# Optimization experiments

Measured on AMD Instinct MI355X. Metric: run time of the kernel, lower is better.

The kernel has to match this reference:

```python
import jax, jax.numpy as jnp
import numpy as np

N, E, G, ND, H, C, L = 100000, 640000, 1000, 128, 128, 10, 4
ATOMS_PER_GRAPH = 100  # N = G * ATOMS_PER_GRAPH
NEG_SLOPE = 0.01  # nn.LeakyReLU default


def setup_inputs() -> dict:
    key = jax.random.key(0)
    ks = jax.random.split(key, 16)
    s = 0.05
    return {
        "node_attr": jax.random.normal(ks[0], (N, ND), jnp.float32),
        "edge_index": jax.random.randint(ks[1], (2, E), 0, N, jnp.int64),
        "num_atoms": jnp.full((G,), ATOMS_PER_GRAPH, dtype=jnp.int64),
        "enc_W": jax.random.normal(ks[2], (ND, H), jnp.float32) * s,
        "enc_b": jnp.zeros((H,), jnp.float32),
        "gcn_W": jax.random.normal(ks[3], (L, H, H), jnp.float32) * s,
        "gcn_b": jnp.zeros((L, H), jnp.float32),
        "r_W1": jax.random.normal(ks[4], (H, H), jnp.float32) * s,
        "r_b1": jnp.zeros((H,), jnp.float32),
        "r_W2": jax.random.normal(ks[5], (H, H), jnp.float32) * s,
        "r_b2": jnp.zeros((H,), jnp.float32),
        "s_W1": jax.random.normal(ks[6], (H, H), jnp.float32) * s,
        "s_b1": jnp.zeros((H,), jnp.float32),
        "s_W2": jax.random.normal(ks[7], (H, H), jnp.float32) * s,
        "s_b2": jnp.zeros((H,), jnp.float32),
        "fin_W": jax.random.normal(ks[8], (H, C), jnp.float32) * s,
        "fin_b": jnp.zeros((C,), jnp.float32),
    }


def _leaky(x):
    return jnp.where(x > 0, x, NEG_SLOPE * x)


def reference(node_attr, edge_index, num_atoms, enc_W, enc_b, gcn_W, gcn_b,
              r_W1, r_b1, r_W2, r_b2, s_W1, s_b1, s_W2, s_b2, fin_W, fin_b):
    dst, src = edge_index[0], edge_index[1]
    # degree normalization constant across layers: deg(i) = in-edge count, divide by deg+1
    deg = jax.ops.segment_sum(jnp.ones((E,), node_attr.dtype), dst, num_segments=N)
    inv_deg = 1.0 / (deg + 1.0)  # [N]

    x = node_attr @ enc_W + enc_b  # [N, H]
    for l in range(L):
        h = x @ gcn_W[l] + gcn_b[l]
        agg = jax.ops.segment_sum(h[src], dst, num_segments=N)  # scatter_sum over dst
        x = (h + agg) * inv_deg[:, None]

    # GateMLP: ReLuMLP(x) * SigmoidMLP(x)
    r = _leaky(_leaky(x @ r_W1 + r_b1) @ r_W2 + r_b2)
    g = jax.nn.sigmoid(_leaky(x @ s_W1 + s_b1) @ s_W2 + s_b2)
    x = r * g  # [N, H]

    # graph pooling: scatter_mean over graph ids
    graph_mask = jnp.repeat(jnp.arange(G), num_atoms, total_repeat_length=N)
    gsum = jax.ops.segment_sum(x, graph_mask, num_segments=G)
    cnt = jax.ops.segment_sum(jnp.ones((N,), x.dtype), graph_mask, num_segments=G)
    graph_attr = gsum / jnp.maximum(cnt, 1.0)[:, None]  # [G, H]
    return graph_attr @ fin_W + fin_b  # [G, C]
```

## Files before the change

kernel.cpp:

```cpp
#include <hip/hip_runtime.h>
#include <hip/hip_bf16.h>
#include <cstddef>
#include <cstdint>

#define CAP 40
#define LEAK 0.01f

typedef __attribute__((ext_vector_type(8))) short short8v;
typedef __attribute__((ext_vector_type(4))) float float4v;

__device__ __forceinline__ unsigned short f2bf(float f) {
    uint32_t u = __float_as_uint(f);
    uint32_t r = (u + 0x7FFFu + ((u >> 16) & 1u)) >> 16;
    return (unsigned short)r;
}
__device__ __forceinline__ float bf2f(unsigned short s) {
    return __uint_as_float(((uint32_t)s) << 16);
}
__device__ __forceinline__ short8v frag_from_pairs(uint32_t p0, uint32_t p1,
                                                   uint32_t p2, uint32_t p3) {
    union { uint32_t u[4]; short8v v; } c;
    c.u[0] = p0; c.u[1] = p1; c.u[2] = p2; c.u[3] = p3;
    return c.v;
}

__global__ void build_buckets(const int* __restrict__ ei, int E_,
                              int* __restrict__ cnt, int* __restrict__ bucket) {
    int e = (blockIdx.x * 256 + threadIdx.x) * 4;
    if (e >= E_) return;
    if (e + 4 <= E_) {
        int4 d4 = *(const int4*)&ei[e];
        int4 s4 = *(const int4*)&ei[(size_t)E_ + e];
        int p0 = atomicAdd(&cnt[d4.x], 1);
        int p1 = atomicAdd(&cnt[d4.y], 1);
        int p2 = atomicAdd(&cnt[d4.z], 1);
        int p3 = atomicAdd(&cnt[d4.w], 1);
        if (p0 < CAP) bucket[(size_t)d4.x * CAP + p0] = s4.x;
        if (p1 < CAP) bucket[(size_t)d4.y * CAP + p1] = s4.y;
        if (p2 < CAP) bucket[(size_t)d4.z * CAP + p2] = s4.z;
        if (p3 < CAP) bucket[(size_t)d4.w * CAP + p3] = s4.w;
    } else {
        for (; e < E_; ++e) {
            int d = ei[e], s = ei[(size_t)E_ + e];
            int p = atomicAdd(&cnt[d], 1);
            if (p < CAP) bucket[(size_t)d * CAP + p] = s;
        }
    }
}

__global__ void pack_w(const float* __restrict__ enc, const float* __restrict__ gcn,
                       const float* __restrict__ rw1, const float* __restrict__ rw2,
                       const float* __restrict__ sw1, const float* __restrict__ sw2,
                       unsigned short* __restrict__ p) {
    int m = blockIdx.x >> 3;
    int idx = (blockIdx.x & 7) * 256 + threadIdx.x;
    const float* W;
    switch (m) {
        case 0: W = enc; break;
        case 1: case 2: case 3: case 4: W = gcn + (size_t)(m - 1) * 16384; break;
        case 5: W = rw1; break;
        case 6: W = rw2; break;
        case 7: W = sw1; break;
        default: W = sw2; break;
    }
    int n = idx & 127;
    int fg = (idx >> 7) & 3;
    int kc = idx >> 9;
    short8v v;
#pragma unroll
    for (int j = 0; j < 8; ++j)
        v[j] = (short)f2bf(W[(size_t)(kc * 32 + fg * 8 + j) * 128 + n]);
    *(short8v*)(p + (size_t)m * 16384 + (size_t)idx * 8) = v;
}

__device__ __forceinline__ void load_wf(const unsigned short* __restrict__ Wpack,
                                        int w, int fr, int fg, short8v wf[2][4]) {
    const short8v* Wp = (const short8v*)Wpack;
#pragma unroll
    for (int t = 0; t < 2; ++t)
#pragma unroll
        for (int kc = 0; kc < 4; ++kc)
            wf[t][kc] = Wp[(kc * 4 + fg) * 128 + w * 32 + t * 16 + fr];
}

__device__ __forceinline__ void mfma_tile(const unsigned short* As, int fr, int fg,
                                          const short8v wf[2][4], float4v acc[4][2]) {
#pragma unroll
    for (int m = 0; m < 4; ++m) {
        acc[m][0] = (float4v){0.f, 0.f, 0.f, 0.f};
        acc[m][1] = (float4v){0.f, 0.f, 0.f, 0.f};
    }
#pragma unroll
    for (int kc = 0; kc < 4; ++kc) {
        short8v a[4];
#pragma unroll
        for (int m = 0; m < 4; ++m) {
            int row = m * 16 + fr;
            int cb = (kc * 64 + fg * 16) ^ ((row & 7) << 4);
            a[m] = *(const short8v*)((const char*)As + row * 256 + cb);
        }
#pragma unroll
        for (int m = 0; m < 4; ++m) {
            acc[m][0] = __builtin_amdgcn_mfma_f32_16x16x32_bf16(a[m], wf[0][kc], acc[m][0], 0, 0, 0);
            acc[m][1] = __builtin_amdgcn_mfma_f32_16x16x32_bf16(a[m], wf[1][kc], acc[m][1], 0, 0, 0);
        }
    }
}

__global__ __launch_bounds__(256) void gemm_enc(const float* __restrict__ Ain,
                                                const unsigned short* __restrict__ Wpack,
                                                const float* __restrict__ bias,
                                                unsigned short* __restrict__ Cout, int M) {
    __shared__ unsigned short As[64 * 128];
    const int tid = threadIdx.x;
    const int lane = tid & 63;
    const int w = tid >> 6;
    const int row0 = blockIdx.x * 64;
    const int fr = lane & 15;
    const int fg = lane >> 4;

    short8v wf[2][4];
    load_wf(Wpack, w, fr, fg, wf);

    {
        const int r = tid >> 2;
        const int cg = tid & 3;
        const int row = row0 + r;
        char* lbase = (char*)As + r * 256;
        const float* Ap = Ain + (size_t)row * 128 + cg * 32;
#pragma unroll
        for (int i = 0; i < 4; ++i) {
            short8v v = {0, 0, 0, 0, 0, 0, 0, 0};
            if (row < M) {
                float4v p = *(const float4v*)(Ap + i * 8);
                float4v q = *(const float4v*)(Ap + i * 8 + 4);
                v[0] = (short)f2bf(p[0]); v[1] = (short)f2bf(p[1]);
                v[2] = (short)f2bf(p[2]); v[3] = (short)f2bf(p[3]);
                v[4] = (short)f2bf(q[0]); v[5] = (short)f2bf(q[1]);
                v[6] = (short)f2bf(q[2]); v[7] = (short)f2bf(q[3]);
            }
            int cb = (cg * 64 + i * 16) ^ ((r & 7) << 4);
            *(short8v*)(lbase + cb) = v;
        }
    }
    __syncthreads();

    float4v acc[4][2];
    mfma_tile(As, fr, fg, wf, acc);

#pragma unroll
    for (int t = 0; t < 2; ++t) {
        const int col = w * 32 + t * 16 + fr;
        const float bv = bias[col];
#pragma unroll
        for (int m = 0; m < 4; ++m)
#pragma unroll
            for (int q = 0; q < 4; ++q) {
                int row = row0 + m * 16 + fg * 4 + q;
                if (row < M) Cout[(size_t)row * 128 + col] = f2bf(acc[m][t][q] + bv);
            }
    }
}

__device__ __forceinline__ void acc8(float a[8], uint4 v, float m) {
    a[0] = fmaf(m, bf2f((unsigned short)(v.x & 0xffff)), a[0]);
    a[1] = fmaf(m, bf2f((unsigned short)(v.x >> 16)), a[1]);
    a[2] = fmaf(m, bf2f((unsigned short)(v.y & 0xffff)), a[2]);
    a[3] = fmaf(m, bf2f((unsigned short)(v.y >> 16)), a[3]);
    a[4] = fmaf(m, bf2f((unsigned short)(v.z & 0xffff)), a[4]);
    a[5] = fmaf(m, bf2f((unsigned short)(v.z >> 16)), a[5]);
    a[6] = fmaf(m, bf2f((unsigned short)(v.w & 0xffff)), a[6]);
    a[7] = fmaf(m, bf2f((unsigned short)(v.w >> 16)), a[7]);
}

__global__ __launch_bounds__(256, 4) void gcn_fused(const unsigned short* __restrict__ x,
                                                    const int* __restrict__ bucket,
                                                    const int* __restrict__ cnt,
                                                    const unsigned short* __restrict__ Wpack,
                                                    const float* __restrict__ bias,
                                                    unsigned short* __restrict__ xout,
                                                    int Nn) {
    __shared__ unsigned short As[64 * 128];
    const int tid = threadIdx.x;
    const int lane = tid & 63;
    const int w = tid >> 6;
    const int row0 = blockIdx.x * 64;
    const int fr = lane & 15;
    const int fg = lane >> 4;
    const int l16 = lane & 15;
    const int g = lane >> 4;
    const int gl = lane & 48;
    const char* xb = (const char*)x;

    int cfull = 0;
    if (lane < 16) {
        int gn = row0 + w * 16 + lane;
        if (gn >= Nn) gn = Nn - 1;
        cfull = cnt[gn];
    }
    uint4 own[4];
    int2 pre[4];
#pragma unroll
    for (int p = 0; p < 4; ++p) {
        int gn = row0 + w * 16 + p * 4 + g;
        if (gn >= Nn) gn = Nn - 1;
        own[p] = *(const uint4*)(xb + (size_t)gn * 256 + l16 * 16);
        pre[p] = *(const int2*)&bucket[(size_t)gn * CAP + 2 * l16];
    }

#pragma unroll
    for (int p = 0; p < 4; ++p) {
        const int n = p * 4 + g;
        const int r = w * 16 + n;
        const int dfull = __shfl(cfull, n);
        const float id = 1.0f / (float)(dfull + 1);
        const int d = min(dfull, CAP);
        const int dm = min(d, 32);

        float a[8];
        {
            uint4 o = own[p];
            a[0] = bf2f((unsigned short)(o.x & 0xffff));
            a[1] = bf2f((unsigned short)(o.x >> 16));
            a[2] = bf2f((unsigned short)(o.y & 0xffff));
            a[3] = bf2f((unsigned short)(o.y >> 16));
            a[4] = bf2f((unsigned short)(o.z & 0xffff));
            a[5] = bf2f((unsigned short)(o.z >> 16));
            a[6] = bf2f((unsigned short)(o.w & 0xffff));
            a[7] = bf2f((unsigned short)(o.w >> 16));
        }

        for (int j = 0; j < dm; j += 4) {
            int sl = gl + (j >> 1);
            int s0 = __shfl(pre[p].x, sl);
            int s1 = __shfl(pre[p].y, sl);
            int s2 = __shfl(pre[p].x, sl + 1);
            int s3 = __shfl(pre[p].y, sl + 1);
            s0 = min(max(s0, 0), Nn - 1);
            s1 = min(max(s1, 0), Nn - 1);
            s2 = min(max(s2, 0), Nn - 1);
            s3 = min(max(s3, 0), Nn - 1);
            uint4 v0 = *(const uint4*)(xb + (size_t)s0 * 256 + l16 * 16);
            uint4 v1 = *(const uint4*)(xb + (size_t)s1 * 256 + l16 * 16);
            uint4 v2 = *(const uint4*)(xb + (size_t)s2 * 256 + l16 * 16);
            uint4 v3 = *(const uint4*)(xb + (size_t)s3 * 256 + l16 * 16);
            acc8(a, v0, (j + 0 < d) ? 1.f : 0.f);
            acc8(a, v1, (j + 1 < d) ? 1.f : 0.f);
            acc8(a, v2, (j + 2 < d) ? 1.f : 0.f);
            acc8(a, v3, (j + 3 < d) ? 1.f : 0.f);
        }
        if (d > 32) {
            int gn = row0 + r; if (gn >= Nn) gn = Nn - 1;
            for (int j = 32; j < d; ++j) {
                int s = bucket[(size_t)gn * CAP + j];
                uint4 v = *(const uint4*)(xb + (size_t)s * 256 + l16 * 16);
                acc8(a, v, 1.f);
            }
        }

#pragma unroll
        for (int i = 0; i < 8; ++i) a[i] *= id;
        uint4 o;
        o.x = (uint32_t)f2bf(a[0]) | ((uint32_t)f2bf(a[1]) << 16);
        o.y = (uint32_t)f2bf(a[2]) | ((uint32_t)f2bf(a[3]) << 16);
        o.z = (uint32_t)f2bf(a[4]) | ((uint32_t)f2bf(a[5]) << 16);
        o.w = (uint32_t)f2bf(a[6]) | ((uint32_t)f2bf(a[7]) << 16);
        *(uint4*)((char*)As + r * 256 + ((l16 * 16) ^ ((r & 7) << 4))) = o;
    }

    short8v wf[2][4];
    load_wf(Wpack, w, fr, fg, wf);
    __syncthreads();

    float4v acc[4][2];
    mfma_tile(As, fr, fg, wf, acc);

#pragma unroll
    for (int t = 0; t < 2; ++t) {
        const int col = w * 32 + t * 16 + fr;
        const float bv = bias[col];
#pragma unroll
        for (int m = 0; m < 4; ++m)
#pragma unroll
            for (int q = 0; q < 4; ++q) {
                int row = row0 + m * 16 + fg * 4 + q;
                if (row < Nn) xout[(size_t)row * 128 + col] = f2bf(acc[m][t][q] + bv);
            }
    }
}

__global__ __launch_bounds__(512, 4) void gate_fused(const unsigned short* __restrict__ x,
                                                     const unsigned short* __restrict__ wpack,
                                                     const float* __restrict__ rb1,
                                                     const float* __restrict__ rb2,
                                                     const float* __restrict__ sb1,
                                                     const float* __restrict__ sb2,
                                                     unsigned short* __restrict__ out, int M) {
    __shared__ unsigned short Ws[2 * 128 * 128];
    const int tid = threadIdx.x;
    const int lane = tid & 63;
    const int w = tid >> 6;
    const int l16 = lane & 15;
    const int fg = lane >> 4;
    const int row0 = blockIdx.x * 128 + w * 16;

    int xr = row0 + l16;
    if (xr >= M) xr = M - 1;
    short8v xbf[4];
#pragma unroll
    for (int kc = 0; kc < 4; ++kc)
        xbf[kc] = *(const short8v*)(x + (size_t)xr * 128 + kc * 32 + fg * 8);

    const short8v* WL = (const short8v*)Ws;
    uint32_t upR[8][2], upS[8][2];

#define STAGE2(mi0, mi1)                                                      \
    {                                                                         \
        const short8v* s0 = (const short8v*)(wpack + (size_t)(mi0) * 16384);  \
        const short8v* s1 = (const short8v*)(wpack + (size_t)(mi1) * 16384);  \
        short8v* dst = (short8v*)Ws;                                          \
        _Pragma("unroll") for (int i = 0; i < 4; ++i)                         \
            dst[i * 512 + tid] = s0[i * 512 + tid];                           \
        _Pragma("unroll") for (int i = 0; i < 4; ++i)                         \
            dst[2048 + i * 512 + tid] = s1[i * 512 + tid];                    \
    }

#define PASS1(OFS, BIAS, UP)                                                  \
    _Pragma("unroll") for (int nt = 0; nt < 8; ++nt) {                        \
        float4v acc = (float4v){0.f, 0.f, 0.f, 0.f};                          \
        _Pragma("unroll") for (int kc = 0; kc < 4; ++kc)                      \
            acc = __builtin_amdgcn_mfma_f32_16x16x32_bf16(                    \
                WL[(OFS) + (kc * 4 + fg) * 128 + nt * 16 + l16], xbf[kc], acc, 0, 0, 0); \
        _Pragma("unroll") for (int q = 0; q < 4; ++q) {                       \
            float v = acc[q] + (BIAS)[nt * 16 + fg * 4 + q];                  \
            acc[q] = v > 0.f ? v : LEAK * v;                                  \
        }                                                                     \
        UP[nt][0] = (uint32_t)f2bf(acc[0]) | ((uint32_t)f2bf(acc[1]) << 16);  \
        UP[nt][1] = (uint32_t)f2bf(acc[2]) | ((uint32_t)f2bf(acc[3]) << 16);  \
    }

#define MKUF(UP, UF)                                                          \
    _Pragma("unroll") for (int kc = 0; kc < 4; ++kc) {                        \
        uint32_t pr0, pr1, pr2, pr3;                                          \
        {                                                                     \
            int srcl = (((2 * fg + 0) & 3) << 4) + l16;                       \
            uint32_t lo = __shfl((int)UP[2 * kc][0], srcl);                   \
            uint32_t hi = __shfl((int)UP[2 * kc + 1][0], srcl);               \
            pr0 = (fg & 2) ? hi : lo;                                         \
            lo = __shfl((int)UP[2 * kc][1], srcl);                            \
            hi = __shfl((int)UP[2 * kc + 1][1], srcl);                        \
            pr1 = (fg & 2) ? hi : lo;                                         \
        }                                                                     \
        {                                                                     \
            int srcl = (((2 * fg + 1) & 3) << 4) + l16;                       \
            uint32_t lo = __shfl((int)UP[2 * kc][0], srcl);                   \
            uint32_t hi = __shfl((int)UP[2 * kc + 1][0], srcl);               \
            pr2 = (fg & 2) ? hi : lo;                                         \
            lo = __shfl((int)UP[2 * kc][1], srcl);                            \
            hi = __shfl((int)UP[2 * kc + 1][1], srcl);                        \
            pr3 = (fg & 2) ? hi : lo;                                         \
        }                                                                     \
        UF[kc] = frag_from_pairs(pr0, pr1, pr2, pr3);                         \
    }

    STAGE2(5, 7);
    __syncthreads();
    PASS1(0, rb1, upR);
    PASS1(2048, sb1, upS);
    __syncthreads();

    STAGE2(6, 8);
    __syncthreads();

    short8v uf[4];
    MKUF(upR, uf);
    float4v rf[8];
#pragma unroll
    for (int t2 = 0; t2 < 8; ++t2) {
        float4v acc = (float4v){0.f, 0.f, 0.f, 0.f};
#pragma unroll
        for (int kc = 0; kc < 4; ++kc)
            acc = __builtin_amdgcn_mfma_f32_16x16x32_bf16(
                uf[kc], WL[(kc * 4 + fg) * 128 + t2 * 16 + l16], acc, 0, 0, 0);
        const float bv = rb2[t2 * 16 + l16];
#pragma unroll
        for (int q = 0; q < 4; ++q) {
            float v = acc[q] + bv;
            rf[t2][q] = v > 0.f ? v : LEAK * v;
        }
    }

    MKUF(upS, uf);
#pragma unroll
    for (int t2 = 0; t2 < 8; ++t2) {
        float4v acc = (float4v){0.f, 0.f, 0.f, 0.f};
#pragma unroll
        for (int kc = 0; kc < 4; ++kc)
            acc = __builtin_amdgcn_mfma_f32_16x16x32_bf16(
                uf[kc], WL[2048 + (kc * 4 + fg) * 128 + t2 * 16 + l16], acc, 0, 0, 0);
        const float bv = sb2[t2 * 16 + l16];
#pragma unroll
        for (int q = 0; q < 4; ++q) {
            int row = row0 + fg * 4 + q;
            if (row < M) {
                float gg = 1.f / (1.f + __expf(-(acc[q] + bv)));
                out[(size_t)row * 128 + t2 * 16 + l16] = f2bf(gg * rf[t2][q]);
            }
        }
    }
#undef STAGE2
#undef PASS1
#undef MKUF
}

__global__ void scan_atoms(const int* __restrict__ na, int* __restrict__ goff, int G_) {
    __shared__ int sh[1024];
    int t = threadIdx.x;
    int v = (t < G_) ? na[t] : 0;
    sh[t] = v;
    __syncthreads();
    for (int ofs = 1; ofs < 1024; ofs <<= 1) {
        int u = (t >= ofs) ? sh[t - ofs] : 0;
        __syncthreads();
        sh[t] += u;
        __syncthreads();
    }
    if (t == 0) goff[0] = 0;
    if (t < G_) goff[t + 1] = sh[t];
}

__global__ void pool(const unsigned short* __restrict__ x, const int* __restrict__ goff,
                     float* __restrict__ gattr, int G_) {
    int g = blockIdx.x * 2 + (threadIdx.x >> 7);
    if (g >= G_) return;
    int d = threadIdx.x & 127;
    int a0 = goff[g], a1 = goff[g + 1];
    float s0 = 0.f, s1 = 0.f, s2 = 0.f, s3 = 0.f;
    int a = a0;
    for (; a + 4 <= a1; a += 4) {
        s0 += bf2f(x[(size_t)(a + 0) * 128 + d]);
        s1 += bf2f(x[(size_t)(a + 1) * 128 + d]);
        s2 += bf2f(x[(size_t)(a + 2) * 128 + d]);
        s3 += bf2f(x[(size_t)(a + 3) * 128 + d]);
    }
    for (; a < a1; ++a) s0 += bf2f(x[(size_t)a * 128 + d]);
    float s = (s0 + s1) + (s2 + s3);
    float c = (float)max(a1 - a0, 1);
    gattr[(size_t)g * 128 + d] = s / c;
}

__global__ void final_gemm(const float* __restrict__ gattr, const float* __restrict__ fW,
                           const float* __restrict__ fb, float* __restrict__ out,
                           int G_, int C_) {
    int i = blockIdx.x * 256 + threadIdx.x;
    if (i >= G_ * C_) return;
    int g = i / C_, c = i % C_;
    const float* row = gattr + (size_t)g * 128;
    float s = fb[c];
    for (int k = 0; k < 128; ++k) s = fmaf(row[k], fW[k * C_ + c], s);
    out[i] = s;
}

extern "C" void kernel_launch(void* const* d_in, const int* in_sizes, int n_in,
                              void* d_out, int out_size, void* d_ws, size_t ws_size,
                              hipStream_t stream) {
    const float* node_attr = (const float*)d_in[0];
    const int* edge_index  = (const int*)d_in[1];
    const int* num_atoms   = (const int*)d_in[2];
    const float* enc_W = (const float*)d_in[3];
    const float* enc_b = (const float*)d_in[4];
    const float* gcn_W = (const float*)d_in[5];
    const float* gcn_b = (const float*)d_in[6];
    const float* r_W1 = (const float*)d_in[7];
    const float* r_b1 = (const float*)d_in[8];
    const float* r_W2 = (const float*)d_in[9];
    const float* r_b2 = (const float*)d_in[10];
    const float* s_W1 = (const float*)d_in[11];
    const float* s_b1 = (const float*)d_in[12];
    const float* s_W2 = (const float*)d_in[13];
    const float* s_b2 = (const float*)d_in[14];
    const float* fin_W = (const float*)d_in[15];
    const float* fin_b = (const float*)d_in[16];
    float* out = (float*)d_out;

    const int N_ = in_sizes[0] / 128;
    const int E_ = in_sizes[1] / 2;
    const int G_ = in_sizes[2];
    const int C_ = in_sizes[16];

    size_t off = 0;
    auto alloc = [&](size_t bytes) -> void* {
        void* p = (char*)d_ws + off;
        off += (bytes + 255) & ~(size_t)255;
        return p;
    };
    unsigned short* bx = (unsigned short*)alloc((size_t)N_ * 128 * 2);
    unsigned short* bh = (unsigned short*)alloc((size_t)N_ * 128 * 2);
    int* bucket = (int*)alloc((size_t)N_ * CAP * 4);
    int* cnt    = (int*)alloc((size_t)N_ * 4);
    unsigned short* wpack = (unsigned short*)alloc((size_t)9 * 16384 * 2);
    int* goff   = (int*)alloc((size_t)(G_ + 1) * 4);
    float* gattr = (float*)alloc((size_t)G_ * 128 * 4);
    (void)ws_size; (void)n_in; (void)out_size;

    const int gemm_grid = (N_ + 63) / 64;

    hipMemsetAsync(cnt, 0, (size_t)N_ * 4, stream);
    build_buckets<<<(E_ / 4 + 255) / 256, 256, 0, stream>>>(edge_index, E_, cnt, bucket);
    pack_w<<<72, 256, 0, stream>>>(enc_W, gcn_W, r_W1, r_W2, s_W1, s_W2, wpack);
    scan_atoms<<<1, 1024, 0, stream>>>(num_atoms, goff, G_);

    gemm_enc<<<gemm_grid, 256, 0, stream>>>(node_attr, wpack, enc_b, bx, N_);

    unsigned short* cur = bx;
    unsigned short* nxt = bh;
    for (int l = 0; l < 4; ++l) {
        gcn_fused<<<gemm_grid, 256, 0, stream>>>(cur, bucket, cnt,
                                                 wpack + (size_t)(1 + l) * 16384,
                                                 gcn_b + (size_t)l * 128, nxt, N_);
        unsigned short* t = cur; cur = nxt; nxt = t;
    }

    gate_fused<<<(N_ + 127) / 128, 512, 0, stream>>>(cur, wpack, r_b1, r_b2, s_b1, s_b2,
                                                     nxt, N_);

    pool<<<(G_ + 1) / 2, 256, 0, stream>>>(nxt, goff, gattr, G_);
    final_gemm<<<(G_ * C_ + 255) / 256, 256, 0, stream>>>(gattr, fin_W, fin_b, out, G_, C_);
}
```

Baseline: 297.5 us.

## Prefetch neighbor gathers across nodes and shrink gate kernel shared memory

```diff
diff --git a/kernel.cpp b/kernel.cpp
--- a/kernel.cpp
+++ b/kernel.cpp
@@ -173,6 +173,26 @@
     a[7] = fmaf(m, bf2f((unsigned short)(v.w >> 16)), a[7]);
 }
 
+__device__ __forceinline__ void issue8(const char* __restrict__ xb, int2 prep,
+                                       int gl, int l16, int Nn, int jb, uint4 V[8]) {
+    const int sl = gl + (jb >> 1);
+    int s[8];
+    s[0] = __shfl(prep.x, sl);     s[1] = __shfl(prep.y, sl);
+    s[2] = __shfl(prep.x, sl + 1); s[3] = __shfl(prep.y, sl + 1);
+    s[4] = __shfl(prep.x, sl + 2); s[5] = __shfl(prep.y, sl + 2);
+    s[6] = __shfl(prep.x, sl + 3); s[7] = __shfl(prep.y, sl + 3);
+#pragma unroll
+    for (int i = 0; i < 8; ++i) {
+        int ss = min(max(s[i], 0), Nn - 1);
+        V[i] = *(const uint4*)(xb + (size_t)ss * 256 + l16 * 16);
+    }
+}
+
+__device__ __forceinline__ void consume8(float a[8], const uint4 V[8], int jb, int d) {
+#pragma unroll
+    for (int i = 0; i < 8; ++i) acc8(a, V[i], (jb + i < d) ? 1.f : 0.f);
+}
+
 __global__ __launch_bounds__(256, 4) void gcn_fused(const unsigned short* __restrict__ x,
                                                     const int* __restrict__ bucket,
                                                     const int* __restrict__ cnt,
@@ -208,65 +228,61 @@
         pre[p] = *(const int2*)&bucket[(size_t)gn * CAP + 2 * l16];
     }
 
-#pragma unroll
-    for (int p = 0; p < 4; ++p) {
-        const int n = p * 4 + g;
-        const int r = w * 16 + n;
-        const int dfull = __shfl(cfull, n);
-        const float id = 1.0f / (float)(dfull + 1);
-        const int d = min(dfull, CAP);
-        const int dm = min(d, 32);
-
-        float a[8];
-        {
-            uint4 o = own[p];
-            a[0] = bf2f((unsigned short)(o.x & 0xffff));
-            a[1] = bf2f((unsigned short)(o.x >> 16));
-            a[2] = bf2f((unsigned short)(o.y & 0xffff));
-            a[3] = bf2f((unsigned short)(o.y >> 16));
-            a[4] = bf2f((unsigned short)(o.z & 0xffff));
-            a[5] = bf2f((unsigned short)(o.z >> 16));
-            a[6] = bf2f((unsigned short)(o.w & 0xffff));
-            a[7] = bf2f((unsigned short)(o.w >> 16));
-        }
-
-        for (int j = 0; j < dm; j += 4) {
-            int sl = gl + (j >> 1);
-            int s0 = __shfl(pre[p].x, sl);
-            int s1 = __shfl(pre[p].y, sl);
-            int s2 = __shfl(pre[p].x, sl + 1);
-            int s3 = __shfl(pre[p].y, sl + 1);
-            s0 = min(max(s0, 0), Nn - 1);
-            s1 = min(max(s1, 0), Nn - 1);
-            s2 = min(max(s2, 0), Nn - 1);
-            s3 = min(max(s3, 0), Nn - 1);
-            uint4 v0 = *(const uint4*)(xb + (size_t)s0 * 256 + l16 * 16);
-            uint4 v1 = *(const uint4*)(xb + (size_t)s1 * 256 + l16 * 16);
-            uint4 v2 = *(const uint4*)(xb + (size_t)s2 * 256 + l16 * 16);
-            uint4 v3 = *(const uint4*)(xb + (size_t)s3 * 256 + l16 * 16);
-            acc8(a, v0, (j + 0 < d) ? 1.f : 0.f);
-            acc8(a, v1, (j + 1 < d) ? 1.f : 0.f);
-            acc8(a, v2, (j + 2 < d) ? 1.f : 0.f);
-            acc8(a, v3, (j + 3 < d) ? 1.f : 0.f);
-        }
-        if (d > 32) {
-            int gn = row0 + r; if (gn >= Nn) gn = Nn - 1;
-            for (int j = 32; j < d; ++j) {
-                int s = bucket[(size_t)gn * CAP + j];
-                uint4 v = *(const uint4*)(xb + (size_t)s * 256 + l16 * 16);
-                acc8(a, v, 1.f);
-            }
-        }
-
-#pragma unroll
-        for (int i = 0; i < 8; ++i) a[i] *= id;
-        uint4 o;
-        o.x = (uint32_t)f2bf(a[0]) | ((uint32_t)f2bf(a[1]) << 16);
-        o.y = (uint32_t)f2bf(a[2]) | ((uint32_t)f2bf(a[3]) << 16);
-        o.z = (uint32_t)f2bf(a[4]) | ((uint32_t)f2bf(a[5]) << 16);
-        o.w = (uint32_t)f2bf(a[6]) | ((uint32_t)f2bf(a[7]) << 16);
-        *(uint4*)((char*)As + r * 256 + ((l16 * 16) ^ ((r & 7) << 4))) = o;
-    }
+    uint4 VA[8], VB[8];
+
+#define DO_PASS(P, V)                                                          \
+    {                                                                          \
+        const int n = (P) * 4 + g;                                             \
+        const int r = w * 16 + n;                                              \
+        const int dfull = __shfl(cfull, n);                                    \
+        const float id = 1.0f / (float)(dfull + 1);                            \
+        const int d = min(dfull, CAP);                                         \
+        float a[8];                                                            \
+        {                                                                      \
+            uint4 o = own[P];                                                  \
+            a[0] = bf2f((unsigned short)(o.x & 0xffff));                       \
+            a[1] = bf2f((unsigned short)(o.x >> 16));                          \
+            a[2] = bf2f((unsigned short)(o.y & 0xffff));                       \
+            a[3] = bf2f((unsigned short)(o.y >> 16));                          \
+            a[4] = bf2f((unsigned short)(o.z & 0xffff));                       \
+            a[5] = bf2f((unsigned short)(o.z >> 16));                          \
+            a[6] = bf2f((unsigned short)(o.w & 0xffff));                       \
+            a[7] = bf2f((unsigned short)(o.w >> 16));                          \
+        }                                                                      \
+        consume8(a, V, 0, d);                                                  \
+        if (d > 8) {                                                           \
+            const int dm = min(d, 32);                                         \
+            for (int jb = 8; jb < dm; jb += 8) {                               \
+                issue8(xb, pre[P], gl, l16, Nn, jb, V);                        \
+                consume8(a, V, jb, d);                                         \
+            }                                                                  \
+            if (d > 32) {                                                      \
+                int gn = row0 + r; if (gn >= Nn) gn = Nn - 1;                  \
+                for (int j = 32; j < d; ++j) {                                 \
+                    int s = bucket[(size_t)gn * CAP + j];                      \
+                    uint4 v = *(const uint4*)(xb + (size_t)s * 256 + l16 * 16);\
+                    acc8(a, v, 1.f);                                           \
+                }                                                              \
+            }                                                                  \
+        }                                                                      \
+        _Pragma("unroll") for (int i = 0; i < 8; ++i) a[i] *= id;              \
+        uint4 o;                                                               \
+        o.x = (uint32_t)f2bf(a[0]) | ((uint32_t)f2bf(a[1]) << 16);             \
+        o.y = (uint32_t)f2bf(a[2]) | ((uint32_t)f2bf(a[3]) << 16);             \
+        o.z = (uint32_t)f2bf(a[4]) | ((uint32_t)f2bf(a[5]) << 16);             \
+        o.w = (uint32_t)f2bf(a[6]) | ((uint32_t)f2bf(a[7]) << 16);             \
+        *(uint4*)((char*)As + r * 256 + ((l16 * 16) ^ ((r & 7) << 4))) = o;    \
+    }
+
+    issue8(xb, pre[0], gl, l16, Nn, 0, VA);
+    issue8(xb, pre[1], gl, l16, Nn, 0, VB);
+    DO_PASS(0, VA);
+    issue8(xb, pre[2], gl, l16, Nn, 0, VA);
+    DO_PASS(1, VB);
+    issue8(xb, pre[3], gl, l16, Nn, 0, VB);
+    DO_PASS(2, VA);
+    DO_PASS(3, VB);
+#undef DO_PASS
 
     short8v wf[2][4];
     load_wf(Wpack, w, fr, fg, wf);
@@ -296,13 +312,12 @@
                                                      const float* __restrict__ sb1,
                                                      const float* __restrict__ sb2,
                                                      unsigned short* __restrict__ out, int M) {
-    __shared__ unsigned short Ws[2 * 128 * 128];
+    __shared__ unsigned short Ws[128 * 128];
     const int tid = threadIdx.x;
     const int lane = tid & 63;
-    const int w = tid >> 6;
     const int l16 = lane & 15;
     const int fg = lane >> 4;
-    const int row0 = blockIdx.x * 128 + w * 16;
+    const int row0 = blockIdx.x * 128 + (tid >> 6) * 16;
 
     int xr = row0 + l16;
     if (xr >= M) xr = M - 1;
@@ -314,23 +329,20 @@
     const short8v* WL = (const short8v*)Ws;
     uint32_t upR[8][2], upS[8][2];
 
-#define STAGE2(mi0, mi1)                                                      \
+#define STAGE(mi)                                                             \
     {                                                                         \
-        const short8v* s0 = (const short8v*)(wpack + (size_t)(mi0) * 16384);  \
-        const short8v* s1 = (const short8v*)(wpack + (size_t)(mi1) * 16384);  \
+        const short8v* src = (const short8v*)(wpack + (size_t)(mi) * 16384);  \
         short8v* dst = (short8v*)Ws;                                          \
         _Pragma("unroll") for (int i = 0; i < 4; ++i)                         \
-            dst[i * 512 + tid] = s0[i * 512 + tid];                           \
-        _Pragma("unroll") for (int i = 0; i < 4; ++i)                         \
-            dst[2048 + i * 512 + tid] = s1[i * 512 + tid];                    \
-    }
-
-#define PASS1(OFS, BIAS, UP)                                                  \
+            dst[i * 512 + tid] = src[i * 512 + tid];                          \
+    }
+
+#define PASS1(BIAS, UP)                                                       \
     _Pragma("unroll") for (int nt = 0; nt < 8; ++nt) {                        \
         float4v acc = (float4v){0.f, 0.f, 0.f, 0.f};                          \
         _Pragma("unroll") for (int kc = 0; kc < 4; ++kc)                      \
             acc = __builtin_amdgcn_mfma_f32_16x16x32_bf16(                    \
-                WL[(OFS) + (kc * 4 + fg) * 128 + nt * 16 + l16], xbf[kc], acc, 0, 0, 0); \
+                WL[(kc * 4 + fg) * 128 + nt * 16 + l16], xbf[kc], acc, 0, 0, 0); \
         _Pragma("unroll") for (int q = 0; q < 4; ++q) {                       \
             float v = acc[q] + (BIAS)[nt * 16 + fg * 4 + q];                  \
             acc[q] = v > 0.f ? v : LEAK * v;                                  \
@@ -363,14 +375,16 @@
         UF[kc] = frag_from_pairs(pr0, pr1, pr2, pr3);                         \
     }
 
-    STAGE2(5, 7);
+    STAGE(5);
     __syncthreads();
-    PASS1(0, rb1, upR);
-    PASS1(2048, sb1, upS);
+    PASS1(rb1, upR);
     __syncthreads();
-
-    STAGE2(6, 8);
+    STAGE(7);
     __syncthreads();
+    PASS1(sb1, upS);
+
+    const short8v* W2R = (const short8v*)(wpack + (size_t)6 * 16384);
+    const short8v* W2S = (const short8v*)(wpack + (size_t)8 * 16384);
 
     short8v uf[4];
     MKUF(upR, uf);
@@ -381,7 +395,7 @@
 #pragma unroll
         for (int kc = 0; kc < 4; ++kc)
             acc = __builtin_amdgcn_mfma_f32_16x16x32_bf16(
-                uf[kc], WL[(kc * 4 + fg) * 128 + t2 * 16 + l16], acc, 0, 0, 0);
+                uf[kc], W2R[(kc * 4 + fg) * 128 + t2 * 16 + l16], acc, 0, 0, 0);
         const float bv = rb2[t2 * 16 + l16];
 #pragma unroll
         for (int q = 0; q < 4; ++q) {
@@ -397,7 +411,7 @@
 #pragma unroll
         for (int kc = 0; kc < 4; ++kc)
             acc = __builtin_amdgcn_mfma_f32_16x16x32_bf16(
-                uf[kc], WL[2048 + (kc * 4 + fg) * 128 + t2 * 16 + l16], acc, 0, 0, 0);
+                uf[kc], W2S[(kc * 4 + fg) * 128 + t2 * 16 + l16], acc, 0, 0, 0);
         const float bv = sb2[t2 * 16 + l16];
 #pragma unroll
         for (int q = 0; q < 4; ++q) {
@@ -408,7 +422,7 @@
             }
         }
     }
-#undef STAGE2
+#undef STAGE
 #undef PASS1
 #undef MKUF
 }
```

After: 376.5 us. +26.6%, slower.

## Read gate MLP weights directly from global memory instead of LDS staging

Applied to the files above, without the earlier changes.

```diff
diff --git a/kernel.cpp b/kernel.cpp
--- a/kernel.cpp
+++ b/kernel.cpp
@@ -289,20 +289,18 @@
     }
 }
 
-__global__ __launch_bounds__(512, 4) void gate_fused(const unsigned short* __restrict__ x,
+__global__ __launch_bounds__(256, 4) void gate_fused(const unsigned short* __restrict__ x,
                                                      const unsigned short* __restrict__ wpack,
                                                      const float* __restrict__ rb1,
                                                      const float* __restrict__ rb2,
                                                      const float* __restrict__ sb1,
                                                      const float* __restrict__ sb2,
                                                      unsigned short* __restrict__ out, int M) {
-    __shared__ unsigned short Ws[2 * 128 * 128];
     const int tid = threadIdx.x;
     const int lane = tid & 63;
-    const int w = tid >> 6;
     const int l16 = lane & 15;
     const int fg = lane >> 4;
-    const int row0 = blockIdx.x * 128 + w * 16;
+    const int row0 = blockIdx.x * 64 + (tid >> 6) * 16;
 
     int xr = row0 + l16;
     if (xr >= M) xr = M - 1;
@@ -311,104 +309,96 @@
     for (int kc = 0; kc < 4; ++kc)
         xbf[kc] = *(const short8v*)(x + (size_t)xr * 128 + kc * 32 + fg * 8);
 
-    const short8v* WL = (const short8v*)Ws;
-    uint32_t upR[8][2], upS[8][2];
-
-#define STAGE2(mi0, mi1)                                                      \
-    {                                                                         \
-        const short8v* s0 = (const short8v*)(wpack + (size_t)(mi0) * 16384);  \
-        const short8v* s1 = (const short8v*)(wpack + (size_t)(mi1) * 16384);  \
-        short8v* dst = (short8v*)Ws;                                          \
-        _Pragma("unroll") for (int i = 0; i < 4; ++i)                         \
-            dst[i * 512 + tid] = s0[i * 512 + tid];                           \
-        _Pragma("unroll") for (int i = 0; i < 4; ++i)                         \
-            dst[2048 + i * 512 + tid] = s1[i * 512 + tid];                    \
-    }
-
-#define PASS1(OFS, BIAS, UP)                                                  \
+    const short8v* W1R = (const short8v*)(wpack + (size_t)5 * 16384);
+    const short8v* W2R = (const short8v*)(wpack + (size_t)6 * 16384);
+    const short8v* W1S = (const short8v*)(wpack + (size_t)7 * 16384);
+    const short8v* W2S = (const short8v*)(wpack + (size_t)8 * 16384);
+
+    uint32_t up[8][2];
+    short8v uf[4];
+
+#define PASS1(WP, BIAS)                                                       \
     _Pragma("unroll") for (int nt = 0; nt < 8; ++nt) {                        \
         float4v acc = (float4v){0.f, 0.f, 0.f, 0.f};                          \
         _Pragma("unroll") for (int kc = 0; kc < 4; ++kc)                      \
             acc = __builtin_amdgcn_mfma_f32_16x16x32_bf16(                    \
-                WL[(OFS) + (kc * 4 + fg) * 128 + nt * 16 + l16], xbf[kc], acc, 0, 0, 0); \
+                (WP)[(kc * 4 + fg) * 128 + nt * 16 + l16], xbf[kc], acc, 0, 0, 0); \
         _Pragma("unroll") for (int q = 0; q < 4; ++q) {                       \
             float v = acc[q] + (BIAS)[nt * 16 + fg * 4 + q];                  \
             acc[q] = v > 0.f ? v : LEAK * v;                                  \
         }                                                                     \
-        UP[nt][0] = (uint32_t)f2bf(acc[0]) | ((uint32_t)f2bf(acc[1]) << 16);  \
-        UP[nt][1] = (uint32_t)f2bf(acc[2]) | ((uint32_t)f2bf(acc[3]) << 16);  \
-    }
-
-#define MKUF(UP, UF)                                                          \
+        up[nt][0] = (uint32_t)f2bf(acc[0]) | ((uint32_t)f2bf(acc[1]) << 16);  \
+        up[nt][1] = (uint32_t)f2bf(acc[2]) | ((uint32_t)f2bf(acc[3]) << 16);  \
+    }
+
+#define MKUF()                                                                \
     _Pragma("unroll") for (int kc = 0; kc < 4; ++kc) {                        \
         uint32_t pr0, pr1, pr2, pr3;                                          \
         {                                                                     \
             int srcl = (((2 * fg + 0) & 3) << 4) + l16;                       \
-            uint32_t lo = __shfl((int)UP[2 * kc][0], srcl);                   \
-            uint32_t hi = __shfl((int)UP[2 * kc + 1][0], srcl);               \
+            uint32_t lo = __shfl((int)up[2 * kc][0], srcl);                   \
+            uint32_t hi = __shfl((int)up[2 * kc + 1][0], srcl);               \
             pr0 = (fg & 2) ? hi : lo;                                         \
-            lo = __shfl((int)UP[2 * kc][1], srcl);                            \
-            hi = __shfl((int)UP[2 * kc + 1][1], srcl);                        \
+            lo = __shfl((int)up[2 * kc][1], srcl);                            \
+            hi = __shfl((int)up[2 * kc + 1][1], srcl);                        \
             pr1 = (fg & 2) ? hi : lo;                                         \
         }                                                                     \
         {                                                                     \
             int srcl = (((2 * fg + 1) & 3) << 4) + l16;                       \
-            uint32_t lo = __shfl((int)UP[2 * kc][0], srcl);                   \
-            uint32_t hi = __shfl((int)UP[2 * kc + 1][0], srcl);               \
+            uint32_t lo = __shfl((int)up[2 * kc][0], srcl);                   \
+            uint32_t hi = __shfl((int)up[2 * kc + 1][0], srcl);               \
             pr2 = (fg & 2) ? hi : lo;                                         \
-            lo = __shfl((int)UP[2 * kc][1], srcl);                            \
-            hi = __shfl((int)UP[2 * kc + 1][1], srcl);                        \
+            lo = __shfl((int)up[2 * kc][1], srcl);                            \
+            hi = __shfl((int)up[2 * kc + 1][1], srcl);                        \
             pr3 = (fg & 2) ? hi : lo;                                         \
         }                                                                     \
-        UF[kc] = frag_from_pairs(pr0, pr1, pr2, pr3);                         \
-    }
-
-    STAGE2(5, 7);
-    __syncthreads();
-    PASS1(0, rb1, upR);
-    PASS1(2048, sb1, upS);
-    __syncthreads();
-
-    STAGE2(6, 8);
-    __syncthreads();
-
-    short8v uf[4];
-    MKUF(upR, uf);
-    float4v rf[8];
+        uf[kc] = frag_from_pairs(pr0, pr1, pr2, pr3);                         \
+    }
+
+    PASS1(W1R, rb1);
+    MKUF();
+    uint32_t rfp[8][2];
 #pragma unroll
     for (int t2 = 0; t2 < 8; ++t2) {
         float4v acc = (float4v){0.f, 0.f, 0.f, 0.f};
 #pragma unroll
         for (int kc = 0; kc < 4; ++kc)
             acc = __builtin_amdgcn_mfma_f32_16x16x32_bf16(
-                uf[kc], WL[(kc * 4 + fg) * 128 + t2 * 16 + l16], acc, 0, 0, 0);
+                uf[kc], W2R[(kc * 4 + fg) * 128 + t2 * 16 + l16], acc, 0, 0, 0);
         const float bv = rb2[t2 * 16 + l16];
 #pragma unroll
         for (int q = 0; q < 4; ++q) {
             float v = acc[q] + bv;
-            rf[t2][q] = v > 0.f ? v : LEAK * v;
-        }
-    }
-
-    MKUF(upS, uf);
+            acc[q] = v > 0.f ? v : LEAK * v;
+        }
+        rfp[t2][0] = (uint32_t)f2bf(acc[0]) | ((uint32_t)f2bf(acc[1]) << 16);
+        rfp[t2][1] = (uint32_t)f2bf(acc[2]) | ((uint32_t)f2bf(acc[3]) << 16);
+    }
+
+    PASS1(W1S, sb1);
+    MKUF();
 #pragma unroll
     for (int t2 = 0; t2 < 8; ++t2) {
         float4v acc = (float4v){0.f, 0.f, 0.f, 0.f};
 #pragma unroll
         for (int kc = 0; kc < 4; ++kc)
             acc = __builtin_amdgcn_mfma_f32_16x16x32_bf16(
-                uf[kc], WL[2048 + (kc * 4 + fg) * 128 + t2 * 16 + l16], acc, 0, 0, 0);
+                uf[kc], W2S[(kc * 4 + fg) * 128 + t2 * 16 + l16], acc, 0, 0, 0);
         const float bv = sb2[t2 * 16 + l16];
+        float r0 = bf2f((unsigned short)(rfp[t2][0] & 0xffff));
+        float r1 = bf2f((unsigned short)(rfp[t2][0] >> 16));
+        float r2 = bf2f((unsigned short)(rfp[t2][1] & 0xffff));
+        float r3 = bf2f((unsigned short)(rfp[t2][1] >> 16));
+        float rr[4] = {r0, r1, r2, r3};
 #pragma unroll
         for (int q = 0; q < 4; ++q) {
             int row = row0 + fg * 4 + q;
             if (row < M) {
                 float gg = 1.f / (1.f + __expf(-(acc[q] + bv)));
-                out[(size_t)row * 128 + t2 * 16 + l16] = f2bf(gg * rf[t2][q]);
+                out[(size_t)row * 128 + t2 * 16 + l16] = f2bf(gg * rr[q]);
             }
         }
     }
-#undef STAGE2
 #undef PASS1
 #undef MKUF
 }
@@ -521,8 +511,7 @@
         unsigned short* t = cur; cur = nxt; nxt = t;
     }
 
-    gate_fused<<<(N_ + 127) / 128, 512, 0, stream>>>(cur, wpack, r_b1, r_b2, s_b1, s_b2,
-                                                     nxt, N_);
+    gate_fused<<<gemm_grid, 256, 0, stream>>>(cur, wpack, r_b1, r_b2, s_b1, s_b2, nxt, N_);
 
     pool<<<(G_ + 1) / 2, 256, 0, stream>>>(nxt, goff, gattr, G_);
     final_gemm<<<(G_ * C_ + 255) / 256, 256, 0, stream>>>(gattr, fin_W, fin_b, out, G_, C_);
```

After: 317.9 us. +6.9%, slower.

## Fuse gate MLP into final GCN layer kernel

Applied to the files above, without the earlier changes.

```diff
diff --git a/kernel.cpp b/kernel.cpp
--- a/kernel.cpp
+++ b/kernel.cpp
@@ -173,14 +173,21 @@
     a[7] = fmaf(m, bf2f((unsigned short)(v.w >> 16)), a[7]);
 }
 
+template <bool GATE>
 __global__ __launch_bounds__(256, 4) void gcn_fused(const unsigned short* __restrict__ x,
                                                     const int* __restrict__ bucket,
                                                     const int* __restrict__ cnt,
                                                     const unsigned short* __restrict__ Wpack,
                                                     const float* __restrict__ bias,
+                                                    const unsigned short* __restrict__ gw,
+                                                    const float* __restrict__ rb1,
+                                                    const float* __restrict__ rb2,
+                                                    const float* __restrict__ sb1,
+                                                    const float* __restrict__ sb2,
                                                     unsigned short* __restrict__ xout,
                                                     int Nn) {
     __shared__ unsigned short As[64 * 128];
+    __shared__ unsigned short Wg[GATE ? 128 * 128 : 8];
     const int tid = threadIdx.x;
     const int lane = tid & 63;
     const int w = tid >> 6;
@@ -191,6 +198,13 @@
     const int g = lane >> 4;
     const int gl = lane & 48;
     const char* xb = (const char*)x;
+
+    if constexpr (GATE) {
+        const short8v* src = (const short8v*)(gw + (size_t)5 * 16384);
+        short8v* dst = (short8v*)Wg;
+#pragma unroll
+        for (int i = 0; i < 8; ++i) dst[i * 256 + tid] = src[i * 256 + tid];
+    }
 
     int cfull = 0;
     if (lane < 16) {
@@ -275,71 +289,65 @@
     float4v acc[4][2];
     mfma_tile(As, fr, fg, wf, acc);
 
-#pragma unroll
-    for (int t = 0; t < 2; ++t) {
-        const int col = w * 32 + t * 16 + fr;
-        const float bv = bias[col];
-#pragma unroll
-        for (int m = 0; m < 4; ++m)
-#pragma unroll
-            for (int q = 0; q < 4; ++q) {
-                int row = row0 + m * 16 + fg * 4 + q;
-                if (row < Nn) xout[(size_t)row * 128 + col] = f2bf(acc[m][t][q] + bv);
-            }
-    }
-}
-
-__global__ __launch_bounds__(512, 4) void gate_fused(const unsigned short* __restrict__ x,
-                                                     const unsigned short* __restrict__ wpack,
-                                                     const float* __restrict__ rb1,
-                                                     const float* __restrict__ rb2,
-                                                     const float* __restrict__ sb1,
-                                                     const float* __restrict__ sb2,
-                                                     unsigned short* __restrict__ out, int M) {
-    __shared__ unsigned short Ws[2 * 128 * 128];
-    const int tid = threadIdx.x;
-    const int lane = tid & 63;
-    const int w = tid >> 6;
-    const int l16 = lane & 15;
-    const int fg = lane >> 4;
-    const int row0 = blockIdx.x * 128 + w * 16;
-
-    int xr = row0 + l16;
-    if (xr >= M) xr = M - 1;
-    short8v xbf[4];
-#pragma unroll
-    for (int kc = 0; kc < 4; ++kc)
-        xbf[kc] = *(const short8v*)(x + (size_t)xr * 128 + kc * 32 + fg * 8);
-
-    const short8v* WL = (const short8v*)Ws;
-    uint32_t upR[8][2], upS[8][2];
-
-#define STAGE2(mi0, mi1)                                                      \
-    {                                                                         \
-        const short8v* s0 = (const short8v*)(wpack + (size_t)(mi0) * 16384);  \
-        const short8v* s1 = (const short8v*)(wpack + (size_t)(mi1) * 16384);  \
-        short8v* dst = (short8v*)Ws;                                          \
-        _Pragma("unroll") for (int i = 0; i < 4; ++i)                         \
-            dst[i * 512 + tid] = s0[i * 512 + tid];                           \
-        _Pragma("unroll") for (int i = 0; i < 4; ++i)                         \
-            dst[2048 + i * 512 + tid] = s1[i * 512 + tid];                    \
-    }
-
-#define PASS1(OFS, BIAS, UP)                                                  \
+    if constexpr (!GATE) {
+#pragma unroll
+        for (int t = 0; t < 2; ++t) {
+            const int col = w * 32 + t * 16 + fr;
+            const float bv = bias[col];
+#pragma unroll
+            for (int m = 0; m < 4; ++m)
+#pragma unroll
+                for (int q = 0; q < 4; ++q) {
+                    int row = row0 + m * 16 + fg * 4 + q;
+                    if (row < Nn) xout[(size_t)row * 128 + col] = f2bf(acc[m][t][q] + bv);
+                }
+        }
+    } else {
+        __syncthreads();
+#pragma unroll
+        for (int t = 0; t < 2; ++t) {
+            const int col = w * 32 + t * 16 + fr;
+            const float bv = bias[col];
+#pragma unroll
+            for (int m = 0; m < 4; ++m)
+#pragma unroll
+                for (int q = 0; q < 4; ++q) {
+                    int r_ = m * 16 + fg * 4 + q;
+                    *(unsigned short*)((char*)As + r_ * 256 +
+                                       ((col * 2) ^ ((r_ & 7) << 4))) =
+                        f2bf(acc[m][t][q] + bv);
+                }
+        }
+        __syncthreads();
+
+        const int r16 = w * 16 + l16;
+        short8v xbf[4];
+#pragma unroll
+        for (int kc = 0; kc < 4; ++kc) {
+            int cb = (kc * 64 + fg * 16) ^ ((r16 & 7) << 4);
+            xbf[kc] = *(const short8v*)((const char*)As + r16 * 256 + cb);
+        }
+        const int row0g = row0 + w * 16;
+        const short8v* WgL = (const short8v*)Wg;
+
+        uint32_t upR[8][2], upS[8][2];
+        short8v uf[4];
+
+#define PASS1(BIAS, UP)                                                       \
     _Pragma("unroll") for (int nt = 0; nt < 8; ++nt) {                        \
-        float4v acc = (float4v){0.f, 0.f, 0.f, 0.f};                          \
+        float4v pacc = (float4v){0.f, 0.f, 0.f, 0.f};                         \
         _Pragma("unroll") for (int kc = 0; kc < 4; ++kc)                      \
-            acc = __builtin_amdgcn_mfma_f32_16x16x32_bf16(                    \
-                WL[(OFS) + (kc * 4 + fg) * 128 + nt * 16 + l16], xbf[kc], acc, 0, 0, 0); \
+            pacc = __builtin_amdgcn_mfma_f32_16x16x32_bf16(                   \
+                WgL[(kc * 4 + fg) * 128 + nt * 16 + l16], xbf[kc], pacc, 0, 0, 0); \
         _Pragma("unroll") for (int q = 0; q < 4; ++q) {                       \
-            float v = acc[q] + (BIAS)[nt * 16 + fg * 4 + q];                  \
-            acc[q] = v > 0.f ? v : LEAK * v;                                  \
+            float v = pacc[q] + (BIAS)[nt * 16 + fg * 4 + q];                 \
+            pacc[q] = v > 0.f ? v : LEAK * v;                                 \
         }                                                                     \
-        UP[nt][0] = (uint32_t)f2bf(acc[0]) | ((uint32_t)f2bf(acc[1]) << 16);  \
-        UP[nt][1] = (uint32_t)f2bf(acc[2]) | ((uint32_t)f2bf(acc[3]) << 16);  \
-    }
-
-#define MKUF(UP, UF)                                                          \
+        UP[nt][0] = (uint32_t)f2bf(pacc[0]) | ((uint32_t)f2bf(pacc[1]) << 16);\
+        UP[nt][1] = (uint32_t)f2bf(pacc[2]) | ((uint32_t)f2bf(pacc[3]) << 16);\
+    }
+
+#define MKUF(UP)                                                              \
     _Pragma("unroll") for (int kc = 0; kc < 4; ++kc) {                        \
         uint32_t pr0, pr1, pr2, pr3;                                          \
         {                                                                     \
@@ -360,57 +368,68 @@
             hi = __shfl((int)UP[2 * kc + 1][1], srcl);                        \
             pr3 = (fg & 2) ? hi : lo;                                         \
         }                                                                     \
-        UF[kc] = frag_from_pairs(pr0, pr1, pr2, pr3);                         \
-    }
-
-    STAGE2(5, 7);
-    __syncthreads();
-    PASS1(0, rb1, upR);
-    PASS1(2048, sb1, upS);
-    __syncthreads();
-
-    STAGE2(6, 8);
-    __syncthreads();
-
-    short8v uf[4];
-    MKUF(upR, uf);
-    float4v rf[8];
-#pragma unroll
-    for (int t2 = 0; t2 < 8; ++t2) {
-        float4v acc = (float4v){0.f, 0.f, 0.f, 0.f};
-#pragma unroll
-        for (int kc = 0; kc < 4; ++kc)
-            acc = __builtin_amdgcn_mfma_f32_16x16x32_bf16(
-                uf[kc], WL[(kc * 4 + fg) * 128 + t2 * 16 + l16], acc, 0, 0, 0);
-        const float bv = rb2[t2 * 16 + l16];
-#pragma unroll
-        for (int q = 0; q < 4; ++q) {
-            float v = acc[q] + bv;
-            rf[t2][q] = v > 0.f ? v : LEAK * v;
-        }
-    }
-
-    MKUF(upS, uf);
-#pragma unroll
-    for (int t2 = 0; t2 < 8; ++t2) {
-        float4v acc = (float4v){0.f, 0.f, 0.f, 0.f};
-#pragma unroll
-        for (int kc = 0; kc < 4; ++kc)
-            acc = __builtin_amdgcn_mfma_f32_16x16x32_bf16(
-                uf[kc], WL[2048 + (kc * 4 + fg) * 128 + t2 * 16 + l16], acc, 0, 0, 0);
-        const float bv = sb2[t2 * 16 + l16];
-#pragma unroll
-        for (int q = 0; q < 4; ++q) {
-            int row = row0 + fg * 4 + q;
-            if (row < M) {
-                float gg = 1.f / (1.f + __expf(-(acc[q] + bv)));
-                out[(size_t)row * 128 + t2 * 16 + l16] = f2bf(gg * rf[t2][q]);
+        uf[kc] = frag_from_pairs(pr0, pr1, pr2, pr3);                         \
+    }
+
+        PASS1(rb1, upR);
+        __syncthreads();
+        {
+            const short8v* src = (const short8v*)(gw + (size_t)7 * 16384);
+            short8v* dst = (short8v*)Wg;
+#pragma unroll
+            for (int i = 0; i < 8; ++i) dst[i * 256 + tid] = src[i * 256 + tid];
+        }
+        __syncthreads();
+        PASS1(sb1, upS);
+
+        const short8v* W2R = (const short8v*)(gw + (size_t)6 * 16384);
+        const short8v* W2S = (const short8v*)(gw + (size_t)8 * 16384);
+
+        MKUF(upR);
+        uint32_t rfp[8][2];
+#pragma unroll
+        for (int t2 = 0; t2 < 8; ++t2) {
+            float4v pacc = (float4v){0.f, 0.f, 0.f, 0.f};
+#pragma unroll
+            for (int kc = 0; kc < 4; ++kc)
+                pacc = __builtin_amdgcn_mfma_f32_16x16x32_bf16(
+                    uf[kc], W2R[(kc * 4 + fg) * 128 + t2 * 16 + l16], pacc, 0, 0, 0);
+            const float bv = rb2[t2 * 16 + l16];
+#pragma unroll
+            for (int q = 0; q < 4; ++q) {
+                float v = pacc[q] + bv;
+                pacc[q] = v > 0.f ? v : LEAK * v;
             }
-        }
-    }
-#undef STAGE2
+            rfp[t2][0] = (uint32_t)f2bf(pacc[0]) | ((uint32_t)f2bf(pacc[1]) << 16);
+            rfp[t2][1] = (uint32_t)f2bf(pacc[2]) | ((uint32_t)f2bf(pacc[3]) << 16);
+        }
+
+        MKUF(upS);
+#pragma unroll
+        for (int t2 = 0; t2 < 8; ++t2) {
+            float4v pacc = (float4v){0.f, 0.f, 0.f, 0.f};
+#pragma unroll
+            for (int kc = 0; kc < 4; ++kc)
+                pacc = __builtin_amdgcn_mfma_f32_16x16x32_bf16(
+                    uf[kc], W2S[(kc * 4 + fg) * 128 + t2 * 16 + l16], pacc, 0, 0, 0);
+            const float bv = sb2[t2 * 16 + l16];
+            float r0 = bf2f((unsigned short)(rfp[t2][0] & 0xffff));
+            float r1 = bf2f((unsigned short)(rfp[t2][0] >> 16));
+            float r2 = bf2f((unsigned short)(rfp[t2][1] & 0xffff));
+            float r3 = bf2f((unsigned short)(rfp[t2][1] >> 16));
+            float rr[4] = {r0, r1, r2, r3};
+#pragma unroll
+            for (int q = 0; q < 4; ++q) {
+                int row = row0g + fg * 4 + q;
+                if (row < Nn) {
+                    float gg = 1.f / (1.f + __expf(-(pacc[q] + bv)));
+                    xout[(size_t)row * 128 + t2 * 16 + l16] = f2bf(gg * rr[q]);
+                }
+            }
+        }
 #undef PASS1
 #undef MKUF
+    }
 }
 
 __global__ void scan_atoms(const int* __restrict__ na, int* __restrict__ goff, int G_) {
@@ -514,15 +533,15 @@
 
     unsigned short* cur = bx;
     unsigned short* nxt = bh;
-    for (int l = 0; l < 4; ++l) {
-        gcn_fused<<<gemm_grid, 256, 0, stream>>>(cur, bucket, cnt,
-                                                 wpack + (size_t)(1 + l) * 16384,
-                                                 gcn_b + (size_t)l * 128, nxt, N_);
+    for (int l = 0; l < 3; ++l) {
+        gcn_fused<false><<<gemm_grid, 256, 0, stream>>>(
+            cur, bucket, cnt, wpack + (size_t)(1 + l) * 16384, gcn_b + (size_t)l * 128,
+            nullptr, nullptr, nullptr, nullptr, nullptr, nxt, N_);
         unsigned short* t = cur; cur = nxt; nxt = t;
     }
-
-    gate_fused<<<(N_ + 127) / 128, 512, 0, stream>>>(cur, wpack, r_b1, r_b2, s_b1, s_b2,
-                                                     nxt, N_);
+    gcn_fused<true><<<gemm_grid, 256, 0, stream>>>(
+        cur, bucket, cnt, wpack + (size_t)4 * 16384, gcn_b + (size_t)3 * 128,
+        wpack, r_b1, r_b2, s_b1, s_b2, nxt, N_);
 
     pool<<<(G_ + 1) / 2, 256, 0, stream>>>(nxt, goff, gattr, G_);
     final_gemm<<<(G_ * C_ + 255) / 256, 256, 0, stream>>>(gattr, fin_W, fin_b, out, G_, C_);
```

After: 312.1 us. +4.9%, slower.
